# Optimization experiments

Measured on AMD Instinct MI355X. Metric: run time of the kernel, lower is better.

## Reference

```python
import jax, jax.numpy as jnp
import numpy as np

B, T, V, E, H = 32, 128, 32000, 300, 512


def setup_inputs() -> dict:
    key = jax.random.key(0)
    ks = jax.random.split(key, 9)
    inputs = jax.random.randint(ks[0], (B, T), 0, V, dtype=jnp.int32)
    hidden = jax.random.normal(ks[1], (B, H), dtype=jnp.float32)
    cell = jax.random.normal(ks[2], (B, H), dtype=jnp.float32)
    # learned params
    emb_table = jax.random.normal(ks[3], (V, E), dtype=jnp.float32) * 0.05
    W_x = jax.random.normal(ks[4], (E, 4 * H), dtype=jnp.float32) * (1.0 / np.sqrt(E))
    W_h = jax.random.normal(ks[5], (H, 4 * H), dtype=jnp.float32) * (1.0 / np.sqrt(H))
    b = jnp.zeros((4 * H,), dtype=jnp.float32)
    W_out = jax.random.normal(ks[6], (H, V), dtype=jnp.float32) * (1.0 / np.sqrt(H))
    b_out = jnp.zeros((V,), dtype=jnp.float32)
    return {"inputs": inputs, "hidden": hidden, "cell": cell,
            "emb_table": emb_table, "W_x": W_x, "W_h": W_h, "b": b,
            "W_out": W_out, "b_out": b_out}


def reference(inputs, hidden, cell, emb_table, W_x, W_h, b, W_out, b_out):
    # Embedding lookup: [B, T, E]
    x = emb_table[inputs]
    # Precompute input-to-gate projection for all timesteps: [B, T, 4H]
    xz = jnp.einsum('bte,eg->btg', x, W_x) + b

    def step(carry, xz_t):
        h, c = carry
        z = xz_t + h @ W_h  # [B, 4H]
        i, f, g, o = jnp.split(z, 4, axis=-1)  # Keras gate order: i, f, c(g), o
        c_new = jax.nn.sigmoid(f) * c + jax.nn.sigmoid(i) * jnp.tanh(g)
        h_new = jax.nn.sigmoid(o) * jnp.tanh(c_new)
        return (h_new, c_new), h_new

    (h_last, c_last), hs = jax.lax.scan(step, (hidden, cell), jnp.swapaxes(xz, 0, 1))
    hs = jnp.swapaxes(hs, 0, 1)  # [B, T, H]
    # TimeDistributed Dense (no activation): [B, T, V]
    logits = jnp.einsum('bth,hv->btv', hs, W_out) + b_out
    return logits, h_last, c_last
```

## Files before the change

### kernel.cpp

```cpp
#include <hip/hip_runtime.h>
#include <cstdint>

using u16 = unsigned short;
using ull = unsigned long long;
typedef __bf16 bf16x8 __attribute__((ext_vector_type(8)));
typedef float  f32x4  __attribute__((ext_vector_type(4)));
typedef float  f32x16 __attribute__((ext_vector_type(16)));

#define DEV __device__ __forceinline__

static constexpr size_t OFF_XZ    = 0;
static constexpr size_t OFF_AEMB  = 33554432;
static constexpr size_t OFF_WXT   = 36175872;
static constexpr size_t OFF_WOT   = 37486592;
static constexpr size_t OFF_WHHI  = 70254592;
static constexpr size_t OFF_WHLO  = 72351744;
static constexpr size_t OFF_HS    = 74448896;
static constexpr size_t OFF_HXHI  = 78643200;
static constexpr size_t OFF_HXLO  = 78708736;
static constexpr size_t OFF_BAR   = 78774272;

DEV u16 f2bf(float x) {
  union { float f; uint32_t u; } v; v.f = x;
  uint32_t r = v.u + 0x7fffu + ((v.u >> 16) & 1u);
  return (u16)(r >> 16);
}
DEV float bf2f(u16 h) { union { uint32_t u; float f; } v; v.u = ((uint32_t)h) << 16; return v.f; }
DEV float sigf(float x)  { return 1.f / (1.f + __expf(-x)); }
DEV float tanh_(float x) { return 2.f / (1.f + __expf(-2.f * x)) - 1.f; }

DEV f32x4 mfma16(bf16x8 a, bf16x8 b, f32x4 c) {
  return __builtin_amdgcn_mfma_f32_16x16x32_bf16(a, b, c, 0, 0, 0);
}
DEV f32x16 mfma32(bf16x8 a, bf16x8 b, f32x16 c) {
  return __builtin_amdgcn_mfma_f32_32x32x16_bf16(a, b, c, 0, 0, 0);
}
DEV void gl_lds16(const u16* g, u16* l) {
  __builtin_amdgcn_global_load_lds(
      (const __attribute__((address_space(1))) uint32_t*)g,
      (__attribute__((address_space(3))) uint32_t*)l, 16, 0, 0);
}


__global__ __launch_bounds__(256) void prep_aemb(const int* __restrict__ toks,
                                                 const float* __restrict__ emb,
                                                 u16* __restrict__ A) {
  int m = blockIdx.x;
  int tok = toks[m];
  const float* src = emb + (size_t)tok * 300;
  for (int k = threadIdx.x; k < 320; k += 256)
    A[(size_t)m * 320 + k] = (k < 300) ? f2bf(src[k]) : (u16)0;
}

__global__ __launch_bounds__(256) void transpose_cvt(const float* __restrict__ in,
                                                     u16* __restrict__ out,
                                                     int K, int N, int Kp) {
  __shared__ float tile[64][65];
  int kt = blockIdx.x * 64, nt = blockIdx.y * 64;
  int c = threadIdx.x & 63, r0 = threadIdx.x >> 6;
  for (int rr = 0; rr < 64; rr += 4) {
    int k = kt + rr + r0;
    tile[rr + r0][c] = (k < K) ? in[(size_t)k * N + nt + c] : 0.f;
  }
  __syncthreads();
  for (int rr = 0; rr < 64; rr += 4) {
    int n = nt + rr + r0;
    out[(size_t)n * Kp + kt + c] = f2bf(tile[c][rr + r0]);
  }
}

__global__ __launch_bounds__(256) void prep_whfrag(const float* __restrict__ Wh,
                                                   u16* __restrict__ hi, u16* __restrict__ lo) {
  int gid = blockIdx.x * 256 + threadIdx.x;
  int l = gid & 63, s = (gid >> 6) & 31, gw = gid >> 11;
  int g = gw >> 2, w = gw & 3;
  int kin  = s * 16 + ((l >> 5) << 3);
  int jcol = w * 512 + g * 32 + (l & 31);
  u16* ph = hi + (size_t)gid * 8;
  u16* pl = lo + (size_t)gid * 8;
#pragma unroll
  for (int i = 0; i < 8; i++) {
    float v = Wh[(size_t)(kin + i) * 2048 + jcol];
    u16 h = f2bf(v);
    ph[i] = h;
    pl[i] = f2bf(v - bf2f(h));
  }
}

__global__ __launch_bounds__(256) void prep_hinit(const float* __restrict__ h0,
                                                  u16* __restrict__ hx_hi, u16* __restrict__ hx_lo) {
  int idx = blockIdx.x * 256 + threadIdx.x;
  int b = idx >> 9, k = idx & 511;
  float v = h0[idx];
  u16 h = f2bf(v);
  int chunk = (k >> 4) * 64 + b * 2 + ((k >> 3) & 1);
  int pos = chunk * 8 + (k & 7);
  hx_hi[pos] = h;
  hx_lo[pos] = f2bf(v - bf2f(h));
}

__global__ __launch_bounds__(256, 2) void gemm_bt(const u16* __restrict__ A, int lda,
                                                  const u16* __restrict__ Bt, int ldb,
                                                  float* __restrict__ C, int ldc,
                                                  const float* __restrict__ bias, int K) {
  __shared__ u16 As[8192];
  __shared__ u16 Bs[8192];
  const int tid = threadIdx.x, lane = tid & 63, wave = tid >> 6;
  const int m0 = blockIdx.y * 128, n0 = blockIdx.x * 128;
  const int wm = (wave >> 1) * 64, wn = (wave & 1) * 64;
  f32x4 acc[4][4];
#pragma unroll
  for (int i = 0; i < 4; i++)
#pragma unroll
    for (int j = 0; j < 4; j++)
#pragma unroll
      for (int r = 0; r < 4; r++) acc[i][j][r] = 0.f;

  const int qbase = wave * 4 * 64 + lane;
  for (int k0 = 0; k0 < K; k0 += 64) {
    __syncthreads();
#pragma unroll
    for (int ii = 0; ii < 4; ii++) {
      int q = qbase + ii * 64;
      int mm = q & 127, kb = q >> 7;
      gl_lds16(A  + (size_t)(m0 + mm) * lda + k0 + kb * 8, As + (size_t)(wave * 4 + ii) * 512);
      gl_lds16(Bt + (size_t)(n0 + mm) * ldb + k0 + kb * 8, Bs + (size_t)(wave * 4 + ii) * 512);
    }
    __syncthreads();
#pragma unroll
    for (int kk = 0; kk < 2; kk++) {
      const int kb  = kk * 4 + (lane >> 4);
      const int row = lane & 15;
      bf16x8 af[4], bfr[4];
#pragma unroll
      for (int s = 0; s < 4; s++) {
        af[s]  = *(const bf16x8*)(As + (size_t)(kb * 128 + wm + s * 16 + row) * 8);
        bfr[s] = *(const bf16x8*)(Bs + (size_t)(kb * 128 + wn + s * 16 + row) * 8);
      }
#pragma unroll
      for (int i = 0; i < 4; i++)
#pragma unroll
        for (int j = 0; j < 4; j++)
          acc[i][j] = mfma16(af[i], bfr[j], acc[i][j]);
    }
  }
  const int coln = lane & 15, rquad = lane >> 4;
#pragma unroll
  for (int j = 0; j < 4; j++) {
    int n = n0 + wn + j * 16 + coln;
    float bv = bias[n];
#pragma unroll
    for (int i = 0; i < 4; i++) {
      int mb = m0 + wm + i * 16 + rquad * 4;
#pragma unroll
      for (int r = 0; r < 4; r++)
        C[(size_t)(mb + r) * ldc + n] = acc[i][j][r] + bv;
    }
  }
}

__global__ __launch_bounds__(256, 1) void lstm_rec(
    const float* __restrict__ xz, const float* __restrict__ cell_in,
    u16* __restrict__ hx_hi, u16* __restrict__ hx_lo, u16* __restrict__ hs,
    const u16* __restrict__ whhi, const u16* __restrict__ whlo,
    float* __restrict__ out_h, float* __restrict__ out_c, int* bar) {
  __shared__ __align__(16) u16 Ah[16384];
  __shared__ __align__(16) u16 Al[16384];
  __shared__ float zb[4][32][32];
  __shared__ float ctile[1024];
  const int tid = threadIdx.x, lane = tid & 63, wave = tid >> 6;
  const int g = blockIdx.x;
  for (int p = tid; p < 1024; p += 256) {
    int b = p >> 5, ko = p & 31;
    ctile[p] = cell_in[b * 512 + g * 32 + ko];
  }
  const int jcol = wave * 512 + g * 32 + (lane & 31);
  const u16* bhib = whhi + (size_t)(g * 4 + wave) * 16384 + lane * 8;
  const u16* blob = whlo + (size_t)(g * 4 + wave) * 16384 + lane * 8;
  bf16x8 Bh[32], Bl[32];
#pragma unroll
  for (int s = 0; s < 32; s++) {
    Bh[s] = *(const bf16x8*)(bhib + (size_t)s * 512);
    Bl[s] = *(const bf16x8*)(blob + (size_t)s * 512);
  }
  const int lchunk = (lane & 31) * 2 + (lane >> 5);
  int brow[16];
#pragma unroll
  for (int r = 0; r < 16; r++) brow[r] = 4 * (lane >> 5) + (r & 3) + 8 * (r >> 2);
  float xzr[16];
#pragma unroll
  for (int r = 0; r < 16; r++) xzr[r] = xz[(size_t)(brow[r] * 128 + 0) * 2048 + jcol];
  const int sb  = tid >> 3;
  const int ko0 = (tid & 7) * 4;
  const int sk0 = g * 32 + ko0;
  const int schunk = (sk0 >> 4) * 64 + sb * 2 + ((sk0 >> 3) & 1);
  const int sull = schunk * 2 + ((sk0 >> 2) & 1);
  ull* hxh = (ull*)hx_hi;
  ull* hxl = (ull*)hx_lo;

  for (int t = 0; t < 128; t++) {
    const ull* ph = hxh + (size_t)(t & 1) * 4096;
    const ull* pl = hxl + (size_t)(t & 1) * 4096;
    ull vh[16], vl[16];
#pragma unroll
    for (int i = 0; i < 16; i++)
      vh[i] = __hip_atomic_load(ph + i * 256 + tid, __ATOMIC_RELAXED, __HIP_MEMORY_SCOPE_AGENT);
#pragma unroll
    for (int i = 0; i < 16; i++)
      vl[i] = __hip_atomic_load(pl + i * 256 + tid, __ATOMIC_RELAXED, __HIP_MEMORY_SCOPE_AGENT);
#pragma unroll
    for (int i = 0; i < 16; i++) ((ull*)Ah)[i * 256 + tid] = vh[i];
#pragma unroll
    for (int i = 0; i < 16; i++) ((ull*)Al)[i * 256 + tid] = vl[i];
    __syncthreads();

    f32x16 acc0, acc1, acc2;
#pragma unroll
    for (int r = 0; r < 16; r++) { acc0[r] = xzr[r]; acc1[r] = 0.f; acc2[r] = 0.f; }
    if (t < 127) {
#pragma unroll
      for (int r = 0; r < 16; r++) xzr[r] = xz[(size_t)(brow[r] * 128 + t + 1) * 2048 + jcol];
    }
#pragma unroll
    for (int s = 0; s < 32; s++) {
      bf16x8 a_hi = *(const bf16x8*)(Ah + s * 512 + lchunk * 8);
      bf16x8 a_lo = *(const bf16x8*)(Al + s * 512 + lchunk * 8);
      acc0 = mfma32(a_hi, Bh[s], acc0);
      acc1 = mfma32(a_hi, Bl[s], acc1);
      acc2 = mfma32(a_lo, Bh[s], acc2);
    }
#pragma unroll
    for (int r = 0; r < 16; r++)
      zb[wave][brow[r]][lane & 31] = acc0[r] + acc1[r] + acc2[r];
    __syncthreads();

    u16 hh[4], hl[4];
    float hv[4], cv[4];
#pragma unroll
    for (int q = 0; q < 4; q++) {
      int ko = ko0 + q, p = sb * 32 + ko;
      float zi = zb[0][sb][ko], zf_ = zb[1][sb][ko], zg = zb[2][sb][ko], zo = zb[3][sb][ko];
      float c = sigf(zf_) * ctile[p] + sigf(zi) * tanh_(zg);
      float h = sigf(zo) * tanh_(c);
      ctile[p] = c;
      hh[q] = f2bf(h);
      hl[q] = f2bf(h - bf2f(hh[q]));
      hv[q] = h; cv[q] = c;
    }
    ull packh = (ull)hh[0] | ((ull)hh[1] << 16) | ((ull)hh[2] << 32) | ((ull)hh[3] << 48);
    ull packl = (ull)hl[0] | ((ull)hl[1] << 16) | ((ull)hl[2] << 32) | ((ull)hl[3] << 48);
    const size_t wbase = (size_t)((t + 1) & 1) * 4096;
    __hip_atomic_store(hxh + wbase + sull, packh, __ATOMIC_RELAXED, __HIP_MEMORY_SCOPE_AGENT);
    __hip_atomic_store(hxl + wbase + sull, packl, __ATOMIC_RELAXED, __HIP_MEMORY_SCOPE_AGENT);
    __hip_atomic_store((ull*)(hs + (size_t)(sb * 128 + t) * 512 + sk0), packh,
                       __ATOMIC_RELAXED, __HIP_MEMORY_SCOPE_AGENT);
    if (t == 127) {
#pragma unroll
      for (int q = 0; q < 4; q++) {
        out_h[sb * 512 + sk0 + q] = hv[q];
        out_c[sb * 512 + sk0 + q] = cv[q];
      }
    }
    __syncthreads();
    if (tid == 0)
      __hip_atomic_store(bar + g * 32, t + 1, __ATOMIC_RELEASE, __HIP_MEMORY_SCOPE_AGENT);
    if (wave == 0 && lane < 16) {
      while (__hip_atomic_load(bar + lane * 32, __ATOMIC_RELAXED, __HIP_MEMORY_SCOPE_AGENT) < t + 1)
        __builtin_amdgcn_s_sleep(1);
    }
    __syncthreads();
  }
}

extern "C" void kernel_launch(void* const* d_in, const int* in_sizes, int n_in,
                              void* d_out, int out_size, void* d_ws, size_t ws_size,
                              hipStream_t stream) {
  const int*   toks = (const int*)d_in[0];
  const float* hid0 = (const float*)d_in[1];
  const float* cel0 = (const float*)d_in[2];
  const float* emb  = (const float*)d_in[3];
  const float* Wx   = (const float*)d_in[4];
  const float* Wh   = (const float*)d_in[5];
  const float* bg   = (const float*)d_in[6];
  const float* Wout = (const float*)d_in[7];
  const float* bout = (const float*)d_in[8];
  float* out = (float*)d_out;
  char* ws = (char*)d_ws;

  float* xz  = (float*)(ws + OFF_XZ);
  u16* aemb  = (u16*)(ws + OFF_AEMB);
  u16* wxT   = (u16*)(ws + OFF_WXT);
  u16* woT   = (u16*)(ws + OFF_WOT);
  u16* whhi  = (u16*)(ws + OFF_WHHI);
  u16* whlo  = (u16*)(ws + OFF_WHLO);
  u16* hs    = (u16*)(ws + OFF_HS);
  u16* hxhi  = (u16*)(ws + OFF_HXHI);
  u16* hxlo  = (u16*)(ws + OFF_HXLO);
  int* bar   = (int*)(ws + OFF_BAR);

  hipMemsetAsync(bar, 0, 4096, stream);
  prep_aemb<<<4096, 256, 0, stream>>>(toks, emb, aemb);
  transpose_cvt<<<dim3(5, 32), 256, 0, stream>>>(Wx, wxT, 300, 2048, 320);
  transpose_cvt<<<dim3(8, 500), 256, 0, stream>>>(Wout, woT, 512, 32000, 512);
  prep_whfrag<<<512, 256, 0, stream>>>(Wh, whhi, whlo);
  prep_hinit<<<64, 256, 0, stream>>>(hid0, hxhi, hxlo);
  gemm_bt<<<dim3(16, 32), 256, 0, stream>>>(aemb, 320, wxT, 320, xz, 2048, bg, 320);
  lstm_rec<<<16, 256, 0, stream>>>(xz, cel0, hxhi, hxlo, hs, whhi, whlo,
                                   out + 131072000, out + 131072000 + 16384, bar);
  gemm_bt<<<dim3(250, 32), 256, 0, stream>>>(hs, 512, woT, 512, out, 32000, bout, 512);
}
```

Before: 1.581 ms.

## Fuse output projection into recurrent kernel, overlapping logits GEMM with recurrence

Merges the LSTM recurrence and the output-vocabulary GEMM into one persistent launch of 256 blocks. Sixteen blocks run the recurrence and publish a per-timestep counter, and the remaining 240 blocks each own a slice of vocabulary columns. Those blocks compute logits for timestep t as soon as h_t is ready, so the large output GEMM overlaps with the serial recurrence instead of running after it. The cost is a small M=32 GEMM per step with repeated weight reads from global memory or cache, spin-wait polling, and a reliance on all 256 blocks being co-resident.

After: 1.893 ms. 19.8% more time.

```diff
diff --git a/kernel.cpp b/kernel.cpp
--- a/kernel.cpp
+++ b/kernel.cpp
@@ -15,7 +15,7 @@
 static constexpr size_t OFF_WOT   = 37486592;
 static constexpr size_t OFF_WHHI  = 70254592;
 static constexpr size_t OFF_WHLO  = 72351744;
-static constexpr size_t OFF_HS    = 74448896;
+static constexpr size_t OFF_HSF   = 74448896;
 static constexpr size_t OFF_HXHI  = 78643200;
 static constexpr size_t OFF_HXLO  = 78708736;
 static constexpr size_t OFF_BAR   = 78774272;
@@ -159,116 +159,194 @@
   }
 }
 
-__global__ __launch_bounds__(256, 1) void lstm_rec(
+__global__ __launch_bounds__(256, 1) void lstm_fused(
     const float* __restrict__ xz, const float* __restrict__ cell_in,
-    u16* __restrict__ hx_hi, u16* __restrict__ hx_lo, u16* __restrict__ hs,
+    u16* __restrict__ hx_hi, u16* __restrict__ hx_lo, ull* __restrict__ hsf,
     const u16* __restrict__ whhi, const u16* __restrict__ whlo,
+    const u16* __restrict__ woT, const float* __restrict__ bout,
+    float* __restrict__ logits,
     float* __restrict__ out_h, float* __restrict__ out_c, int* bar) {
   __shared__ __align__(16) u16 Ah[16384];
   __shared__ __align__(16) u16 Al[16384];
   __shared__ float zb[4][32][32];
   __shared__ float ctile[1024];
   const int tid = threadIdx.x, lane = tid & 63, wave = tid >> 6;
-  const int g = blockIdx.x;
-  for (int p = tid; p < 1024; p += 256) {
-    int b = p >> 5, ko = p & 31;
-    ctile[p] = cell_in[b * 512 + g * 32 + ko];
-  }
-  const int jcol = wave * 512 + g * 32 + (lane & 31);
-  const u16* bhib = whhi + (size_t)(g * 4 + wave) * 16384 + lane * 8;
-  const u16* blob = whlo + (size_t)(g * 4 + wave) * 16384 + lane * 8;
-  bf16x8 Bh[32], Bl[32];
-#pragma unroll
-  for (int s = 0; s < 32; s++) {
-    Bh[s] = *(const bf16x8*)(bhib + (size_t)s * 512);
-    Bl[s] = *(const bf16x8*)(blob + (size_t)s * 512);
-  }
-  const int lchunk = (lane & 31) * 2 + (lane >> 5);
-  int brow[16];
-#pragma unroll
-  for (int r = 0; r < 16; r++) brow[r] = 4 * (lane >> 5) + (r & 3) + 8 * (r >> 2);
-  float xzr[16];
-#pragma unroll
-  for (int r = 0; r < 16; r++) xzr[r] = xz[(size_t)(brow[r] * 128 + 0) * 2048 + jcol];
-  const int sb  = tid >> 3;
-  const int ko0 = (tid & 7) * 4;
-  const int sk0 = g * 32 + ko0;
-  const int schunk = (sk0 >> 4) * 64 + sb * 2 + ((sk0 >> 3) & 1);
-  const int sull = schunk * 2 + ((sk0 >> 2) & 1);
-  ull* hxh = (ull*)hx_hi;
-  ull* hxl = (ull*)hx_lo;
-
-  for (int t = 0; t < 128; t++) {
-    const ull* ph = hxh + (size_t)(t & 1) * 4096;
-    const ull* pl = hxl + (size_t)(t & 1) * 4096;
-    ull vh[16], vl[16];
-#pragma unroll
-    for (int i = 0; i < 16; i++)
-      vh[i] = __hip_atomic_load(ph + i * 256 + tid, __ATOMIC_RELAXED, __HIP_MEMORY_SCOPE_AGENT);
-#pragma unroll
-    for (int i = 0; i < 16; i++)
-      vl[i] = __hip_atomic_load(pl + i * 256 + tid, __ATOMIC_RELAXED, __HIP_MEMORY_SCOPE_AGENT);
-#pragma unroll
-    for (int i = 0; i < 16; i++) ((ull*)Ah)[i * 256 + tid] = vh[i];
-#pragma unroll
-    for (int i = 0; i < 16; i++) ((ull*)Al)[i * 256 + tid] = vl[i];
-    __syncthreads();
-
-    f32x16 acc0, acc1, acc2;
-#pragma unroll
-    for (int r = 0; r < 16; r++) { acc0[r] = xzr[r]; acc1[r] = 0.f; acc2[r] = 0.f; }
-    if (t < 127) {
-#pragma unroll
-      for (int r = 0; r < 16; r++) xzr[r] = xz[(size_t)(brow[r] * 128 + t + 1) * 2048 + jcol];
-    }
+
+  if (blockIdx.x < 16) {
+    const int g = blockIdx.x;
+    for (int p = tid; p < 1024; p += 256) {
+      int b = p >> 5, ko = p & 31;
+      ctile[p] = cell_in[b * 512 + g * 32 + ko];
+    }
+    const int jcol = wave * 512 + g * 32 + (lane & 31);
+    const u16* bhib = whhi + (size_t)(g * 4 + wave) * 16384 + lane * 8;
+    const u16* blob = whlo + (size_t)(g * 4 + wave) * 16384 + lane * 8;
+    bf16x8 Bh[32], Bl[32];
 #pragma unroll
     for (int s = 0; s < 32; s++) {
-      bf16x8 a_hi = *(const bf16x8*)(Ah + s * 512 + lchunk * 8);
-      bf16x8 a_lo = *(const bf16x8*)(Al + s * 512 + lchunk * 8);
-      acc0 = mfma32(a_hi, Bh[s], acc0);
-      acc1 = mfma32(a_hi, Bl[s], acc1);
-      acc2 = mfma32(a_lo, Bh[s], acc2);
-    }
-#pragma unroll
-    for (int r = 0; r < 16; r++)
-      zb[wave][brow[r]][lane & 31] = acc0[r] + acc1[r] + acc2[r];
-    __syncthreads();
-
-    u16 hh[4], hl[4];
-    float hv[4], cv[4];
-#pragma unroll
-    for (int q = 0; q < 4; q++) {
-      int ko = ko0 + q, p = sb * 32 + ko;
-      float zi = zb[0][sb][ko], zf_ = zb[1][sb][ko], zg = zb[2][sb][ko], zo = zb[3][sb][ko];
-      float c = sigf(zf_) * ctile[p] + sigf(zi) * tanh_(zg);
-      float h = sigf(zo) * tanh_(c);
-      ctile[p] = c;
-      hh[q] = f2bf(h);
-      hl[q] = f2bf(h - bf2f(hh[q]));
-      hv[q] = h; cv[q] = c;
-    }
-    ull packh = (ull)hh[0] | ((ull)hh[1] << 16) | ((ull)hh[2] << 32) | ((ull)hh[3] << 48);
-    ull packl = (ull)hl[0] | ((ull)hl[1] << 16) | ((ull)hl[2] << 32) | ((ull)hl[3] << 48);
-    const size_t wbase = (size_t)((t + 1) & 1) * 4096;
-    __hip_atomic_store(hxh + wbase + sull, packh, __ATOMIC_RELAXED, __HIP_MEMORY_SCOPE_AGENT);
-    __hip_atomic_store(hxl + wbase + sull, packl, __ATOMIC_RELAXED, __HIP_MEMORY_SCOPE_AGENT);
-    __hip_atomic_store((ull*)(hs + (size_t)(sb * 128 + t) * 512 + sk0), packh,
-                       __ATOMIC_RELAXED, __HIP_MEMORY_SCOPE_AGENT);
-    if (t == 127) {
+      Bh[s] = *(const bf16x8*)(bhib + (size_t)s * 512);
+      Bl[s] = *(const bf16x8*)(blob + (size_t)s * 512);
+    }
+    const int lchunk = (lane & 31) * 2 + (lane >> 5);
+    int brow[16];
+#pragma unroll
+    for (int r = 0; r < 16; r++) brow[r] = 4 * (lane >> 5) + (r & 3) + 8 * (r >> 2);
+    float xzr[16];
+#pragma unroll
+    for (int r = 0; r < 16; r++) xzr[r] = xz[(size_t)(brow[r] * 128 + 0) * 2048 + jcol];
+    const int sb  = tid >> 3;
+    const int ko0 = (tid & 7) * 4;
+    const int sk0 = g * 32 + ko0;
+    const int schunk = (sk0 >> 4) * 64 + sb * 2 + ((sk0 >> 3) & 1);
+    const int sull = schunk * 2 + ((sk0 >> 2) & 1);
+    ull* hxh = (ull*)hx_hi;
+    ull* hxl = (ull*)hx_lo;
+
+    for (int t = 0; t < 128; t++) {
+      if (g == 0 && tid == 0 && t > 0)
+        __hip_atomic_store(bar + 512, t, __ATOMIC_RELEASE, __HIP_MEMORY_SCOPE_AGENT);
+      const ull* ph = hxh + (size_t)(t & 1) * 4096;
+      const ull* pl = hxl + (size_t)(t & 1) * 4096;
+      ull vh[16], vl[16];
+#pragma unroll
+      for (int i = 0; i < 16; i++)
+        vh[i] = __hip_atomic_load(ph + i * 256 + tid, __ATOMIC_RELAXED, __HIP_MEMORY_SCOPE_AGENT);
+#pragma unroll
+      for (int i = 0; i < 16; i++)
+        vl[i] = __hip_atomic_load(pl + i * 256 + tid, __ATOMIC_RELAXED, __HIP_MEMORY_SCOPE_AGENT);
+#pragma unroll
+      for (int i = 0; i < 16; i++) ((ull*)Ah)[i * 256 + tid] = vh[i];
+#pragma unroll
+      for (int i = 0; i < 16; i++) ((ull*)Al)[i * 256 + tid] = vl[i];
+      __syncthreads();
+
+      f32x16 acc0, acc1, acc2;
+#pragma unroll
+      for (int r = 0; r < 16; r++) { acc0[r] = xzr[r]; acc1[r] = 0.f; acc2[r] = 0.f; }
+      if (t < 127) {
+#pragma unroll
+        for (int r = 0; r < 16; r++) xzr[r] = xz[(size_t)(brow[r] * 128 + t + 1) * 2048 + jcol];
+      }
+#pragma unroll
+      for (int s = 0; s < 32; s++) {
+        bf16x8 a_hi = *(const bf16x8*)(Ah + s * 512 + lchunk * 8);
+        bf16x8 a_lo = *(const bf16x8*)(Al + s * 512 + lchunk * 8);
+        acc0 = mfma32(a_hi, Bh[s], acc0);
+        acc1 = mfma32(a_hi, Bl[s], acc1);
+        acc2 = mfma32(a_lo, Bh[s], acc2);
+      }
+#pragma unroll
+      for (int r = 0; r < 16; r++)
+        zb[wave][brow[r]][lane & 31] = acc0[r] + acc1[r] + acc2[r];
+      __syncthreads();
+
+      u16 hh[4], hl[4];
+      float hv[4], cv[4];
 #pragma unroll
       for (int q = 0; q < 4; q++) {
-        out_h[sb * 512 + sk0 + q] = hv[q];
-        out_c[sb * 512 + sk0 + q] = cv[q];
-      }
-    }
-    __syncthreads();
-    if (tid == 0)
-      __hip_atomic_store(bar + g * 32, t + 1, __ATOMIC_RELEASE, __HIP_MEMORY_SCOPE_AGENT);
-    if (wave == 0 && lane < 16) {
-      while (__hip_atomic_load(bar + lane * 32, __ATOMIC_RELAXED, __HIP_MEMORY_SCOPE_AGENT) < t + 1)
-        __builtin_amdgcn_s_sleep(1);
-    }
-    __syncthreads();
+        int ko = ko0 + q, p = sb * 32 + ko;
+        float zi = zb[0][sb][ko], zf_ = zb[1][sb][ko], zg = zb[2][sb][ko], zo = zb[3][sb][ko];
+        float c = sigf(zf_) * ctile[p] + sigf(zi) * tanh_(zg);
+        float h = sigf(zo) * tanh_(c);
+        ctile[p] = c;
+        hh[q] = f2bf(h);
+        hl[q] = f2bf(h - bf2f(hh[q]));
+        hv[q] = h; cv[q] = c;
+      }
+      ull packh = (ull)hh[0] | ((ull)hh[1] << 16) | ((ull)hh[2] << 32) | ((ull)hh[3] << 48);
+      ull packl = (ull)hl[0] | ((ull)hl[1] << 16) | ((ull)hl[2] << 32) | ((ull)hl[3] << 48);
+      const size_t wbase = (size_t)((t + 1) & 1) * 4096;
+      __hip_atomic_store(hxh + wbase + sull, packh, __ATOMIC_RELAXED, __HIP_MEMORY_SCOPE_AGENT);
+      __hip_atomic_store(hxl + wbase + sull, packl, __ATOMIC_RELAXED, __HIP_MEMORY_SCOPE_AGENT);
+      __hip_atomic_store(hsf + (size_t)t * 4096 + sull, packh,
+                         __ATOMIC_RELAXED, __HIP_MEMORY_SCOPE_AGENT);
+      if (t == 127) {
+#pragma unroll
+        for (int q = 0; q < 4; q++) {
+          out_h[sb * 512 + sk0 + q] = hv[q];
+          out_c[sb * 512 + sk0 + q] = cv[q];
+        }
+      }
+      __syncthreads();
+      if (tid == 0)
+        __hip_atomic_store(bar + g * 32, t + 1, __ATOMIC_RELEASE, __HIP_MEMORY_SCOPE_AGENT);
+      if (wave == 0 && lane < 16) {
+        while (__hip_atomic_load(bar + lane * 32, __ATOMIC_RELAXED, __HIP_MEMORY_SCOPE_AGENT) < t + 1)
+          __builtin_amdgcn_s_sleep(1);
+      }
+      __syncthreads();
+    }
+    if (g == 0 && tid == 0)
+      __hip_atomic_store(bar + 512, 128, __ATOMIC_RELEASE, __HIP_MEMORY_SCOPE_AGENT);
+  } else {
+    const int w = blockIdx.x - 16;
+    const int n00 = w * 128;
+    const bool two = (w < 10);
+    const int n01 = (w + 240) * 128;
+    const int wm16 = (wave & 1) * 16;
+    const int wn   = (wave >> 1) * 64;
+    const int hi = lane >> 4, r15 = lane & 15;
+    const int cbase2 = (((hi >> 1) * 64 + (wm16 + r15) * 2 + (hi & 1))) * 2;
+    const u16* bp0[4]; const u16* bp1[4];
+    float bv0[4], bv1[4];
+#pragma unroll
+    for (int j = 0; j < 4; j++) {
+      int n = n00 + wn + j * 16 + r15;
+      bp0[j] = woT + (size_t)n * 512 + hi * 8;
+      bv0[j] = bout[n];
+      int n1 = n01 + wn + j * 16 + r15;
+      bp1[j] = woT + (size_t)(two ? n1 : n) * 512 + hi * 8;
+      bv1[j] = two ? bout[n1] : 0.f;
+    }
+    const int brow0 = wm16 + hi * 4;
+
+    for (int t = 0; t < 128; t++) {
+      if (wave == 0) {
+        while (__hip_atomic_load(bar + 512, __ATOMIC_RELAXED, __HIP_MEMORY_SCOPE_AGENT) < t + 1)
+          __builtin_amdgcn_s_sleep(8);
+      }
+      __syncthreads();
+      __builtin_amdgcn_sched_barrier(0);
+      const ull* at = hsf + (size_t)t * 4096 + cbase2;
+      ull au0[16], au1[16];
+#pragma unroll
+      for (int kk = 0; kk < 16; kk++) {
+        au0[kk] = __hip_atomic_load(at + kk * 256,     __ATOMIC_RELAXED, __HIP_MEMORY_SCOPE_AGENT);
+        au1[kk] = __hip_atomic_load(at + kk * 256 + 1, __ATOMIC_RELAXED, __HIP_MEMORY_SCOPE_AGENT);
+      }
+      f32x4 acc0[4], acc1[4];
+#pragma unroll
+      for (int j = 0; j < 4; j++)
+#pragma unroll
+        for (int r = 0; r < 4; r++) { acc0[j][r] = 0.f; acc1[j][r] = 0.f; }
+#pragma unroll
+      for (int kk = 0; kk < 16; kk++) {
+        union { ull u[2]; bf16x8 v; } av;
+        av.u[0] = au0[kk]; av.u[1] = au1[kk];
+#pragma unroll
+        for (int j = 0; j < 4; j++) {
+          bf16x8 b0 = *(const bf16x8*)(bp0[j] + kk * 32);
+          acc0[j] = mfma16(av.v, b0, acc0[j]);
+        }
+        if (two) {
+#pragma unroll
+          for (int j = 0; j < 4; j++) {
+            bf16x8 b1 = *(const bf16x8*)(bp1[j] + kk * 32);
+            acc1[j] = mfma16(av.v, b1, acc1[j]);
+          }
+        }
+      }
+#pragma unroll
+      for (int j = 0; j < 4; j++) {
+#pragma unroll
+        for (int r = 0; r < 4; r++) {
+          size_t row = (size_t)(brow0 + r) * 128 + t;
+          logits[row * 32000 + (n00 + wn + j * 16 + r15)] = acc0[j][r] + bv0[j];
+          if (two)
+            logits[row * 32000 + (n01 + wn + j * 16 + r15)] = acc1[j][r] + bv1[j];
+        }
+      }
+    }
   }
 }
 
@@ -293,7 +371,7 @@
   u16* woT   = (u16*)(ws + OFF_WOT);
   u16* whhi  = (u16*)(ws + OFF_WHHI);
   u16* whlo  = (u16*)(ws + OFF_WHLO);
-  u16* hs    = (u16*)(ws + OFF_HS);
+  ull* hsf   = (ull*)(ws + OFF_HSF);
   u16* hxhi  = (u16*)(ws + OFF_HXHI);
   u16* hxlo  = (u16*)(ws + OFF_HXLO);
   int* bar   = (int*)(ws + OFF_BAR);
@@ -305,7 +383,7 @@
   prep_whfrag<<<512, 256, 0, stream>>>(Wh, whhi, whlo);
   prep_hinit<<<64, 256, 0, stream>>>(hid0, hxhi, hxlo);
   gemm_bt<<<dim3(16, 32), 256, 0, stream>>>(aemb, 320, wxT, 320, xz, 2048, bg, 320);
-  lstm_rec<<<16, 256, 0, stream>>>(xz, cel0, hxhi, hxlo, hs, whhi, whlo,
-                                   out + 131072000, out + 131072000 + 16384, bar);
-  gemm_bt<<<dim3(250, 32), 256, 0, stream>>>(hs, 512, woT, 512, out, 32000, bout, 512);
-}
+  lstm_fused<<<256, 256, 0, stream>>>(xz, cel0, hxhi, hxlo, hsf, whhi, whlo,
+                                      woT, bout, out,
+                                      out + 131072000, out + 131072000 + 16384, bar);
+}
```
